# Kernel tuning notes

Hardware: AMD Instinct MI355X
Metric: run time of the kernel (lower is better)

## Reference

```python
import math
import jax
import jax.numpy as jnp
import numpy as np

SEGMENT_SIZE = 2048   # w (init: segment_size)
DILATION_RATE = 4     # r (init: dilation_rate)
D_MODEL = 1024        # init: d_model


def _sparse_indices(n: int, w: int, r: int, head_idx: int) -> np.ndarray:
    """Static SparsifyIndices: per segment of size w, take tokens offset::r.
    Since r divides w, every segment yields exactly m=w//r indices (no -1 pad).
    Returns flat global token indices, shape (S*m,)."""
    S = n // w
    m = w // r
    off = head_idx % r
    seg_start = np.arange(S, dtype=np.int64)[:, None] * w      # (S,1)
    within = off + r * np.arange(m, dtype=np.int64)[None, :]   # (1,m)
    return (seg_start + within).reshape(-1)


def setup_inputs() -> dict:
    key = jax.random.key(0)
    x = jax.random.normal(key, (4, 8192, D_MODEL), dtype=jnp.float32)
    return {"x": x, "head_idx": 1}


def reference(x, head_idx):
    b, n0, d = x.shape
    w, r = SEGMENT_SIZE, DILATION_RATE
    pad = (-n0) % w
    if pad:
        x = jnp.pad(x, ((0, 0), (0, pad), (0, 0)))
    n = n0 + pad
    idx = _sparse_indices(n, w, r, int(head_idx))  # static, (S*m,)
    S, m = n // w, w // r

    # Gather dilated tokens per segment: (b, S, m, d)
    xg = x[:, idx, :].reshape(b, S, m, d)

    # Softmax attention within each sub-segment (q=k=v=xg)
    scores = jnp.einsum('bsid,bsjd->bsij', xg, xg) / math.sqrt(d)  # (b,S,m,m)
    probs = jax.nn.softmax(scores, axis=-1)
    att = jnp.einsum('bsij,bsjd->bsid', probs, xg).reshape(b, S * m, d)

    # MixOutputs: alpha-weighted scatter-add back to full sequence
    denoms = att.sum(-1)                                       # (b, S*m)
    denom_sums = jnp.zeros((b, n), x.dtype).at[:, idx].add(denoms)
    alphas = denoms / denom_sums[:, idx]                       # (b, S*m)
    out = jnp.zeros((b, n, d), x.dtype).at[:, idx, :].add(att * alphas[..., None])
    return out
```

## Files before the change

### kernel.cpp

```cpp
#include <hip/hip_runtime.h>
#include <hip/hip_bf16.h>


typedef __bf16 bf16_t;
typedef __bf16 bf16x8 __attribute__((ext_vector_type(8)));
typedef float floatx4 __attribute__((ext_vector_type(4)));

#define D_MODEL 1024
#define SEG_W   2048
#define RATE    4
#define M_SUB   512
#define NTOK    8192
#define NSEGT   16
#define XG_ELEMS ((long)NSEGT * M_SUB * D_MODEL)

__device__ __forceinline__ void gload16(const bf16_t* g, bf16_t* l) {
    __builtin_amdgcn_global_load_lds(
        (const __attribute__((address_space(1))) void*)g,
        (__attribute__((address_space(3))) void*)l, 16, 0, 0);
}

#define MFMA16(a, b, c) __builtin_amdgcn_mfma_f32_16x16x32_bf16((a), (b), (c), 0, 0, 0)

__global__ __launch_bounds__(256) void gather_kernel(
    const float* __restrict__ x, const int* __restrict__ hidp,
    bf16_t* __restrict__ xg, bf16_t* __restrict__ xgT)
{
    const int off = ((hidp[0] % RATE) + RATE) % RATE;
    const int bid = blockIdx.x;
    const int seg = bid >> 7;
    const int rem = bid & 127;
    const int it  = rem >> 4;
    const int dt  = rem & 15;
    const int b   = seg >> 2, s = seg & 3;

    __shared__ ushort tile[64][65];

    const int t  = threadIdx.x;
    const int r  = t >> 2;
    const int cq = (t & 3) << 4;

    union U8 { bf16x8 v; ushort u[8]; };

    {
        const int  i   = it * 64 + r;
        const long tok = (long)s * SEG_W + off + 4L * i;
        const float* src = x + ((long)b * NTOK + tok) * D_MODEL + dt * 64 + cq;
        float4 f0 = ((const float4*)src)[0];
        float4 f1 = ((const float4*)src)[1];
        float4 f2 = ((const float4*)src)[2];
        float4 f3 = ((const float4*)src)[3];
        U8 lo, hi;
        lo.v[0]=(bf16_t)f0.x; lo.v[1]=(bf16_t)f0.y; lo.v[2]=(bf16_t)f0.z; lo.v[3]=(bf16_t)f0.w;
        lo.v[4]=(bf16_t)f1.x; lo.v[5]=(bf16_t)f1.y; lo.v[6]=(bf16_t)f1.z; lo.v[7]=(bf16_t)f1.w;
        hi.v[0]=(bf16_t)f2.x; hi.v[1]=(bf16_t)f2.y; hi.v[2]=(bf16_t)f2.z; hi.v[3]=(bf16_t)f2.w;
        hi.v[4]=(bf16_t)f3.x; hi.v[5]=(bf16_t)f3.y; hi.v[6]=(bf16_t)f3.z; hi.v[7]=(bf16_t)f3.w;
        bf16_t* dstg = xg + ((long)seg * M_SUB + i) * D_MODEL + dt * 64 + cq;
        *(bf16x8*)(dstg)     = lo.v;
        *(bf16x8*)(dstg + 8) = hi.v;
        #pragma unroll
        for (int j = 0; j < 8; ++j) { tile[r][cq + j] = lo.u[j]; tile[r][cq + 8 + j] = hi.u[j]; }
    }
    __syncthreads();
    {
        const int dc = r;
        const int iq = cq;
        U8 o0, o1;
        #pragma unroll
        for (int j = 0; j < 8; ++j) { o0.u[j] = tile[iq + j][dc]; o1.u[j] = tile[iq + 8 + j][dc]; }
        bf16_t* dstT = xgT + ((long)seg * D_MODEL + dt * 64 + dc) * M_SUB + it * 64 + iq;
        *(bf16x8*)(dstT)     = o0.v;
        *(bf16x8*)(dstT + 8) = o1.v;
    }
}

__global__ __launch_bounds__(512, 2) void attn_kernel(
    const bf16_t* __restrict__ xg, const bf16_t* __restrict__ xgT,
    const int* __restrict__ hidp, float* __restrict__ out)
{
    const int off  = ((hidp[0] % RATE) + RATE) % RATE;
    const int bid0 = blockIdx.x;
    const int sub  = bid0 >> 3;
    const int seg  = (bid0 & 7) * 2 + (sub >> 4);
    const int band = sub & 15;
    const int b = seg >> 2, s = seg & 3;

    const int tid  = threadIdx.x;
    const int w    = tid >> 6;
    const int lane = tid & 63;
    const int l16  = lane & 15;
    const int quad = lane >> 4;

    __shared__ alignas(16) char arena[131072];
    bf16_t* Pl = (bf16_t*)arena;
    float (*redmax)[32] = (float(*)[32])(arena + 98304);
    float (*redsum)[32] = (float(*)[32])(arena + 99328);

    const bf16_t* xs = xg + (long)seg * M_SUB * D_MODEL;

    const bf16_t* qr0 = xs + (long)(band * 32 + l16) * D_MODEL + quad * 8;
    const bf16_t* qr1 = qr0 + 16 * D_MODEL;

    const bf16_t* ksrc = xs + (long)(w * 64 + (lane >> 2)) * D_MODEL
                            + (((lane & 3) ^ (lane >> 4)) * 8);
    auto stageK = [&](int buf, int t) {
        bf16_t* dst = (bf16_t*)arena + buf * 16384 + (w * 64) * 32;
        const bf16_t* src = ksrc + t * 32;
        #pragma unroll
        for (int j = 0; j < 4; ++j)
            gload16(src + j * 16 * D_MODEL, dst + j * 512);
    };

    const bf16_t* vsrc = xgT + ((long)seg * D_MODEL + w * 64 + (lane >> 2)) * M_SUB
                             + (((lane & 3) ^ (lane >> 4)) * 8);
    auto stageV = [&](int buf, int p, int t) {
        bf16_t* dst = (bf16_t*)(arena + 32768) + buf * 16384 + (w * 64) * 32;
        const bf16_t* src = vsrc + (long)p * 512 * M_SUB + t * 32;
        #pragma unroll
        for (int j = 0; j < 4; ++j)
            gload16(src + j * 16 * M_SUB, dst + j * 512);
    };

    const int rsw = (l16 >> 2) & 3;

    floatx4 accS[2][4];
    #pragma unroll
    for (int m = 0; m < 2; ++m)
        #pragma unroll
        for (int n = 0; n < 4; ++n) accS[m][n] = (floatx4){0.f, 0.f, 0.f, 0.f};

    bf16x8 qe0, qe1, qo0, qo1;
    qe0 = *(const bf16x8*)qr0; qe1 = *(const bf16x8*)qr1;
    stageK(0, 0); stageK(1, 1);

    #pragma unroll
    for (int t = 0; t < 32; ++t) {
        if (t == 31) asm volatile("s_waitcnt vmcnt(0)");
        else         asm volatile("s_waitcnt vmcnt(4)");
        __builtin_amdgcn_s_barrier();
        __builtin_amdgcn_sched_barrier(0);

        const bf16_t* Kb = (const bf16_t*)arena + (t % 3) * 16384;
        bf16x8 Bf[4];
        #pragma unroll
        for (int n = 0; n < 4; ++n) {
            const int row = w * 64 + n * 16 + l16;
            Bf[n] = *(const bf16x8*)&Kb[row * 32 + ((quad ^ rsw) * 8)];
        }
        if (t < 31) {
            if (t & 1) { qe0 = *(const bf16x8*)(qr0 + (t + 1) * 32); qe1 = *(const bf16x8*)(qr1 + (t + 1) * 32); }
            else       { qo0 = *(const bf16x8*)(qr0 + (t + 1) * 32); qo1 = *(const bf16x8*)(qr1 + (t + 1) * 32); }
        }
        if (t < 30) stageK((t + 2) % 3, t + 2);

        const bf16x8 A0 = (t & 1) ? qo0 : qe0;
        const bf16x8 A1 = (t & 1) ? qo1 : qe1;
        #pragma unroll
        for (int n = 0; n < 4; ++n) {
            accS[0][n] = MFMA16(A0, Bf[n], accS[0][n]);
            accS[1][n] = MFMA16(A1, Bf[n], accS[1][n]);
        }
    }

    #pragma unroll
    for (int m = 0; m < 2; ++m)
        #pragma unroll
        for (int n = 0; n < 4; ++n)
            #pragma unroll
            for (int rg = 0; rg < 4; ++rg) accS[m][n][rg] *= 0.03125f;

    float mx[2][4];
    #pragma unroll
    for (int m = 0; m < 2; ++m)
        #pragma unroll
        for (int rg = 0; rg < 4; ++rg)
            mx[m][rg] = fmaxf(fmaxf(accS[m][0][rg], accS[m][1][rg]),
                              fmaxf(accS[m][2][rg], accS[m][3][rg]));
    #pragma unroll
    for (int d = 1; d < 16; d <<= 1)
        #pragma unroll
        for (int m = 0; m < 2; ++m)
            #pragma unroll
            for (int rg = 0; rg < 4; ++rg)
                mx[m][rg] = fmaxf(mx[m][rg], __shfl_xor(mx[m][rg], d, 64));
    if (l16 == 0) {
        #pragma unroll
        for (int m = 0; m < 2; ++m)
            #pragma unroll
            for (int rg = 0; rg < 4; ++rg)
                redmax[w][m * 16 + quad * 4 + rg] = mx[m][rg];
    }
    __syncthreads();
    float gm[2][4];
    #pragma unroll
    for (int m = 0; m < 2; ++m)
        #pragma unroll
        for (int rg = 0; rg < 4; ++rg) {
            const int row = m * 16 + quad * 4 + rg;
            float g = redmax[0][row];
            #pragma unroll
            for (int ww = 1; ww < 8; ++ww) g = fmaxf(g, redmax[ww][row]);
            gm[m][rg] = g;
        }
    float sm[2][4] = {{0.f,0.f,0.f,0.f},{0.f,0.f,0.f,0.f}};
    #pragma unroll
    for (int m = 0; m < 2; ++m)
        #pragma unroll
        for (int n = 0; n < 4; ++n)
            #pragma unroll
            for (int rg = 0; rg < 4; ++rg) {
                const float e = __expf(accS[m][n][rg] - gm[m][rg]);
                accS[m][n][rg] = e;
                sm[m][rg] += e;
            }
    #pragma unroll
    for (int d = 1; d < 16; d <<= 1)
        #pragma unroll
        for (int m = 0; m < 2; ++m)
            #pragma unroll
            for (int rg = 0; rg < 4; ++rg)
                sm[m][rg] += __shfl_xor(sm[m][rg], d, 64);
    if (l16 == 0) {
        #pragma unroll
        for (int m = 0; m < 2; ++m)
            #pragma unroll
            for (int rg = 0; rg < 4; ++rg)
                redsum[w][m * 16 + quad * 4 + rg] = sm[m][rg];
    }
    __syncthreads();
    float iv[2][4];
    #pragma unroll
    for (int m = 0; m < 2; ++m)
        #pragma unroll
        for (int rg = 0; rg < 4; ++rg) {
            const int row = m * 16 + quad * 4 + rg;
            float tt = redsum[0][row];
            #pragma unroll
            for (int ww = 1; ww < 8; ++ww) tt += redsum[ww][row];
            iv[m][rg] = 1.f / tt;
        }

    stageV(0, 0, 0); stageV(1, 0, 1);

    #pragma unroll
    for (int m = 0; m < 2; ++m)
        #pragma unroll
        for (int rg = 0; rg < 4; ++rg) {
            const int row = m * 16 + quad * 4 + rg;
            const float f = iv[m][rg];
            #pragma unroll
            for (int n = 0; n < 4; ++n) {
                const int col = w * 64 + n * 16 + l16;
                const int sw  = (((col >> 3) ^ (row & 7)) << 3) + (col & 7);
                Pl[row * 512 + sw] = (bf16_t)(accS[m][n][rg] * f);
            }
        }
    asm volatile("s_waitcnt lgkmcnt(0)");
    __builtin_amdgcn_s_barrier();
    __builtin_amdgcn_sched_barrier(0);

    floatx4 accA[2][4], accB[2][4];
    #pragma unroll
    for (int m = 0; m < 2; ++m)
        #pragma unroll
        for (int n = 0; n < 4; ++n) {
            accA[m][n] = (floatx4){0.f, 0.f, 0.f, 0.f};
            accB[m][n] = (floatx4){0.f, 0.f, 0.f, 0.f};
        }

    auto pv_pass = [&](int p, floatx4 (&acc)[2][4]) {
        #pragma unroll
        for (int t = 0; t < 16; ++t) {
            if (t == 15) asm volatile("s_waitcnt vmcnt(0)");
            else         asm volatile("s_waitcnt vmcnt(4)");
            __builtin_amdgcn_s_barrier();
            __builtin_amdgcn_sched_barrier(0);

            const bf16_t* Vb = (const bf16_t*)(arena + 32768) + (t % 3) * 16384;
            bf16x8 Af[2], Bf[4];
            const int ch = (t * 4 + quad) ^ (l16 & 7);
            #pragma unroll
            for (int m = 0; m < 2; ++m)
                Af[m] = *(const bf16x8*)&Pl[(m * 16 + l16) * 512 + ch * 8];
            #pragma unroll
            for (int n = 0; n < 4; ++n) {
                const int row = w * 64 + n * 16 + l16;
                Bf[n] = *(const bf16x8*)&Vb[row * 32 + ((quad ^ rsw) * 8)];
            }
            if (t < 14) stageV((t + 2) % 3, p, t + 2);
            #pragma unroll
            for (int m = 0; m < 2; ++m)
                #pragma unroll
                for (int n = 0; n < 4; ++n)
                    acc[m][n] = MFMA16(Af[m], Bf[n], acc[m][n]);
        }
    };

    pv_pass(0, accA);
    __builtin_amdgcn_s_barrier();
    __builtin_amdgcn_sched_barrier(0);
    stageV(0, 1, 0); stageV(1, 1, 1);
    pv_pass(1, accB);

    float* obase = out + (long)b * NTOK * D_MODEL;
    #pragma unroll
    for (int m = 0; m < 2; ++m)
        #pragma unroll
        for (int rg = 0; rg < 4; ++rg) {
            const long tok = (long)s * SEG_W + off + 4L * (band * 32 + m * 16 + quad * 4 + rg);
            float* orow = obase + tok * D_MODEL;
            #pragma unroll
            for (int n = 0; n < 4; ++n) {
                const int d = w * 64 + n * 16 + l16;
                __builtin_nontemporal_store(accA[m][n][rg], orow + d);
                __builtin_nontemporal_store(accB[m][n][rg], orow + 512 + d);
            }
        }

    {
        const floatx4 z = {0.f, 0.f, 0.f, 0.f};
        const int chunk = tid & 255;
        const int half  = tid >> 8;
        #pragma unroll 4
        for (int p = 0; p < 48; ++p) {
            const int t = p * 2 + half;
            const int q = t / 3, e = t % 3;
            const int delta = e + (e >= off ? 1 : 0);
            const long tok = (long)s * SEG_W + 4L * (band * 32 + q) + delta;
            __builtin_nontemporal_store(z, (floatx4*)(obase + tok * D_MODEL + chunk * 4));
        }
    }
}

extern "C" void kernel_launch(void* const* d_in, const int* in_sizes, int n_in,
                              void* d_out, int out_size, void* d_ws, size_t ws_size,
                              hipStream_t stream) {
    const float* x   = (const float*)d_in[0];
    const int*   hid = (const int*)d_in[1];
    float*       out = (float*)d_out;
    bf16_t* xg  = (bf16_t*)d_ws;
    bf16_t* xgT = xg + XG_ELEMS;

    gather_kernel<<<dim3(2048), dim3(256), 0, stream>>>(x, hid, xg, xgT);
    attn_kernel<<<dim3(256), dim3(512), 0, stream>>>(xg, xgT, hid, out);
}
```

Before: 263.4 us.

## Deepen K/V/Q prefetch rings and drop per-iteration block barriers

Extends the K staging ring from three to four LDS buffers and prefetches Q fragments three steps ahead. The V ring now keeps three tiles in flight, and each V refill is issued after that step's MFMAs. The s_barrier calls inside the QK and PV loops are removed, which relies on each wave only reading the LDS rows it staged itself. This is meant to cut block-wide sync stalls and hide more global latency, at the cost of more registers and LDS. It also risks subtle WAR or RAW hazards if any cross-wave sharing was missed.

```diff
diff --git a/kernel.cpp b/kernel.cpp
--- a/kernel.cpp
+++ b/kernel.cpp
@@ -91,10 +91,12 @@
     const int l16  = lane & 15;
     const int quad = lane >> 4;
 
-    __shared__ alignas(16) char arena[131072];
-    bf16_t* Pl = (bf16_t*)arena;
-    float (*redmax)[32] = (float(*)[32])(arena + 98304);
-    float (*redsum)[32] = (float(*)[32])(arena + 99328);
+    __shared__ alignas(16) char arena[133120];
+    bf16_t* Kring = (bf16_t*)arena;
+    float (*redmax)[32] = (float(*)[32])(arena + 131072);
+    float (*redsum)[32] = (float(*)[32])(arena + 132096);
+    bf16_t* Pl    = (bf16_t*)arena;
+    bf16_t* Vring = (bf16_t*)(arena + 32768);
 
     const bf16_t* xs = xg + (long)seg * M_SUB * D_MODEL;
 
@@ -104,7 +106,7 @@
     const bf16_t* ksrc = xs + (long)(w * 64 + (lane >> 2)) * D_MODEL
                             + (((lane & 3) ^ (lane >> 4)) * 8);
     auto stageK = [&](int buf, int t) {
-        bf16_t* dst = (bf16_t*)arena + buf * 16384 + (w * 64) * 32;
+        bf16_t* dst = Kring + buf * 16384 + (w * 64) * 32;
         const bf16_t* src = ksrc + t * 32;
         #pragma unroll
         for (int j = 0; j < 4; ++j)
@@ -114,7 +116,7 @@
     const bf16_t* vsrc = xgT + ((long)seg * D_MODEL + w * 64 + (lane >> 2)) * M_SUB
                              + (((lane & 3) ^ (lane >> 4)) * 8);
     auto stageV = [&](int buf, int p, int t) {
-        bf16_t* dst = (bf16_t*)(arena + 32768) + buf * 16384 + (w * 64) * 32;
+        bf16_t* dst = Vring + buf * 16384 + (w * 64) * 32;
         const bf16_t* src = vsrc + (long)p * 512 * M_SUB + t * 32;
         #pragma unroll
         for (int j = 0; j < 4; ++j)
@@ -129,36 +131,36 @@
         #pragma unroll
         for (int n = 0; n < 4; ++n) accS[m][n] = (floatx4){0.f, 0.f, 0.f, 0.f};
 
-    bf16x8 qe0, qe1, qo0, qo1;
-    qe0 = *(const bf16x8*)qr0; qe1 = *(const bf16x8*)qr1;
-    stageK(0, 0); stageK(1, 1);
+    bf16x8 qf[4][2];
+    #pragma unroll
+    for (int p0 = 0; p0 < 3; ++p0) {
+        qf[p0][0] = *(const bf16x8*)(qr0 + p0 * 32);
+        qf[p0][1] = *(const bf16x8*)(qr1 + p0 * 32);
+        stageK(p0, p0);
+    }
 
     #pragma unroll
     for (int t = 0; t < 32; ++t) {
-        if (t == 31) asm volatile("s_waitcnt vmcnt(0)");
-        else         asm volatile("s_waitcnt vmcnt(4)");
-        __builtin_amdgcn_s_barrier();
-        __builtin_amdgcn_sched_barrier(0);
-
-        const bf16_t* Kb = (const bf16_t*)arena + (t % 3) * 16384;
+        if (t <= 29)      asm volatile("s_waitcnt vmcnt(12)" ::: "memory");
+        else if (t == 30) asm volatile("s_waitcnt vmcnt(6)"  ::: "memory");
+        else              asm volatile("s_waitcnt vmcnt(0)"  ::: "memory");
+
+        const bf16_t* Kb = Kring + (t & 3) * 16384;
         bf16x8 Bf[4];
         #pragma unroll
         for (int n = 0; n < 4; ++n) {
             const int row = w * 64 + n * 16 + l16;
             Bf[n] = *(const bf16x8*)&Kb[row * 32 + ((quad ^ rsw) * 8)];
         }
-        if (t < 31) {
-            if (t & 1) { qe0 = *(const bf16x8*)(qr0 + (t + 1) * 32); qe1 = *(const bf16x8*)(qr1 + (t + 1) * 32); }
-            else       { qo0 = *(const bf16x8*)(qr0 + (t + 1) * 32); qo1 = *(const bf16x8*)(qr1 + (t + 1) * 32); }
-        }
-        if (t < 30) stageK((t + 2) % 3, t + 2);
-
-        const bf16x8 A0 = (t & 1) ? qo0 : qe0;
-        const bf16x8 A1 = (t & 1) ? qo1 : qe1;
+        if (t <= 28) {
+            qf[(t + 3) & 3][0] = *(const bf16x8*)(qr0 + (t + 3) * 32);
+            qf[(t + 3) & 3][1] = *(const bf16x8*)(qr1 + (t + 3) * 32);
+            stageK((t + 3) & 3, t + 3);
+        }
         #pragma unroll
         for (int n = 0; n < 4; ++n) {
-            accS[0][n] = MFMA16(A0, Bf[n], accS[0][n]);
-            accS[1][n] = MFMA16(A1, Bf[n], accS[1][n]);
+            accS[0][n] = MFMA16(qf[t & 3][0], Bf[n], accS[0][n]);
+            accS[1][n] = MFMA16(qf[t & 3][1], Bf[n], accS[1][n]);
         }
     }
 
@@ -240,7 +242,7 @@
             iv[m][rg] = 1.f / tt;
         }
 
-    stageV(0, 0, 0); stageV(1, 0, 1);
+    stageV(0, 0, 0); stageV(1, 0, 1); stageV(2, 0, 2);
 
     #pragma unroll
     for (int m = 0; m < 2; ++m)
@@ -255,7 +257,7 @@
                 Pl[row * 512 + sw] = (bf16_t)(accS[m][n][rg] * f);
             }
         }
-    asm volatile("s_waitcnt lgkmcnt(0)");
+    asm volatile("s_waitcnt lgkmcnt(0)" ::: "memory");
     __builtin_amdgcn_s_barrier();
     __builtin_amdgcn_sched_barrier(0);
 
@@ -271,12 +273,11 @@
     auto pv_pass = [&](int p, floatx4 (&acc)[2][4]) {
         #pragma unroll
         for (int t = 0; t < 16; ++t) {
-            if (t == 15) asm volatile("s_waitcnt vmcnt(0)");
-            else         asm volatile("s_waitcnt vmcnt(4)");
-            __builtin_amdgcn_s_barrier();
-            __builtin_amdgcn_sched_barrier(0);
-
-            const bf16_t* Vb = (const bf16_t*)(arena + 32768) + (t % 3) * 16384;
+            if (t <= 13)      asm volatile("s_waitcnt vmcnt(8)" ::: "memory");
+            else if (t == 14) asm volatile("s_waitcnt vmcnt(4)" ::: "memory");
+            else              asm volatile("s_waitcnt vmcnt(0)" ::: "memory");
+
+            const bf16_t* Vb = Vring + (t % 3) * 16384;
             bf16x8 Af[2], Bf[4];
             const int ch = (t * 4 + quad) ^ (l16 & 7);
             #pragma unroll
@@ -287,19 +288,17 @@
                 const int row = w * 64 + n * 16 + l16;
                 Bf[n] = *(const bf16x8*)&Vb[row * 32 + ((quad ^ rsw) * 8)];
             }
-            if (t < 14) stageV((t + 2) % 3, p, t + 2);
             #pragma unroll
             for (int m = 0; m < 2; ++m)
                 #pragma unroll
                 for (int n = 0; n < 4; ++n)
                     acc[m][n] = MFMA16(Af[m], Bf[n], acc[m][n]);
+            if (t <= 12) stageV(t % 3, p, t + 3);
         }
     };
 
     pv_pass(0, accA);
-    __builtin_amdgcn_s_barrier();
-    __builtin_amdgcn_sched_barrier(0);
-    stageV(0, 1, 0); stageV(1, 1, 1);
+    stageV(0, 1, 0); stageV(1, 1, 1); stageV(2, 1, 2);
     pv_pass(1, accB);
 
     float* obase = out + (long)b * NTOK * D_MODEL;
```

After: 253.4 us. -3.8%, faster.
